# Kernel optimization log

Hardware: AMD Instinct MI355X
Metric: run time of the kernel (lower is better)

Reference implementation:

```python
import jax, jax.numpy as jnp
import numpy as np

H = 8       # n_heads
N = 128     # n_vars
HEAD = 64   # per-head dim (== __init__ dim)


def setup_inputs() -> dict:
    key = jax.random.key(0)
    k0, k1, k2, k3, k4 = jax.random.split(key, 5)
    B, L = 4, 8192
    D = H * HEAD
    x = jax.random.normal(k0, (B, L, D), dtype=jnp.float32)
    # nn.Linear default init: U(-1/sqrt(fan_in), 1/sqrt(fan_in)), fan_in = HEAD
    s = 1.0 / np.sqrt(HEAD)
    w1 = jax.random.uniform(k1, (HEAD, HEAD), jnp.float32, -s, s)
    b1 = jax.random.uniform(k2, (HEAD,), jnp.float32, -s, s)
    w2 = jax.random.uniform(k3, (HEAD, HEAD), jnp.float32, -s, s)
    b2 = jax.random.uniform(k4, (HEAD,), jnp.float32, -s, s)
    return {"x": x, "w1": w1, "b1": b1, "w2": w2, "b2": b2}


def reference(x, w1, b1, w2, b2):
    B, L, D = x.shape
    P = L // N  # patches per variable
    # (B,L,D) -> (B,H,L,HEAD) -> (B,H,N,P,HEAD)
    xh = x.reshape(B, L, H, HEAD).transpose(0, 2, 1, 3).reshape(B, H, N, P, HEAD)
    q = xh @ w1.T + b1  # proj_1
    k = xh @ w2.T + b2  # proj_2
    # per (b,h,patch) NxN adjacency over variables
    adj = jax.nn.gelu(jnp.einsum('bhixd,bhjxd->bhxij', q, k), approximate=False)
    adj = jax.nn.softmax(adj, axis=-1)
    # dropout is identity in eval mode; F.normalize(p=1): divide by max(L1, eps)
    adj = adj / jnp.maximum(jnp.sum(jnp.abs(adj), axis=-1, keepdims=True), 1e-12)
    out = jnp.einsum('bhxij,bhjxd->bixhd', adj, xh)  # (B,N,P,H,HEAD)
    return out.reshape(B, L, H * HEAD)
```

## Files before the change

kernel.cpp:

```cpp
#include <hip/hip_runtime.h>
#include <math.h>


namespace {
constexpr int H = 8, NV = 128, HEAD = 64, B = 4, L = 8192;
constexpr int P = L / NV;
constexpr int D = H * HEAD;
constexpr int RS = P * D;
constexpr int NT2 = (B * H * P) / 2;

constexpr int XT_S = 136;
constexpr int XH_S = 72;
constexpr int TA_S = 72;

typedef _Float16 half8  __attribute__((ext_vector_type(8)));
typedef _Float16 half4h __attribute__((ext_vector_type(4)));
typedef _Float16 half2v __attribute__((ext_vector_type(2)));
typedef float    floatx4 __attribute__((ext_vector_type(4)));

__device__ __forceinline__ floatx4 mfma16(half8 a, half8 b, floatx4 c) {
    return __builtin_amdgcn_mfma_f32_16x16x32_f16(a, b, c, 0, 0, 0);
}

__device__ __forceinline__ float& uslot(_Float16* xt, int j) {
    return ((float*)(xt + (j >> 2) * XT_S + 128))[j & 3];
}
__device__ __forceinline__ float& vslot(_Float16* xt, int j) {
    return ((float*)(xt + (32 + (j >> 2)) * XT_S + 128))[j & 3];
}

__global__ __launch_bounds__(256) void pack_g(
    const float* __restrict__ w1, const float* __restrict__ w2,
    const float* __restrict__ b1, const float* __restrict__ b2,
    _Float16* __restrict__ gxh, float* __restrict__ cf)
{
    const int t = threadIdx.x;
    if (blockIdx.x == 16) {
        for (int z = t; z < 14 * 64; z += 256) gxh[66 * 64 + z] = (_Float16)0.f;
        if (t < 64) {
            float a = 0.f;
            #pragma unroll 8
            for (int n = 0; n < 64; ++n) a = fmaf(w2[n * 64 + t], b1[n], a);
            gxh[64 * 64 + t] = (_Float16)a;
        } else if (t < 128) {
            const int d = t - 64;
            float a = 0.f;
            #pragma unroll 8
            for (int n = 0; n < 64; ++n) a = fmaf(w1[n * 64 + d], b2[n], a);
            gxh[65 * 64 + d] = (_Float16)a;
        } else if (t == 128) {
            float a = 0.f;
            for (int n = 0; n < 64; ++n) a = fmaf(b1[n], b2[n], a);
            cf[0] = a;
        }
        return;
    }
    const int gid = blockIdx.x * 256 + t;
    const int d = gid & 63, e = gid >> 6;
    float a = 0.f;
    #pragma unroll 8
    for (int n = 0; n < 64; ++n) a = fmaf(w1[n * 64 + d], w2[n * 64 + e], a);
    gxh[e * 64 + d] = (_Float16)a;
}

__global__ __launch_bounds__(256, 3) void space_graph_mfma9(
    const float* __restrict__ x, const _Float16* __restrict__ gxh,
    const float* __restrict__ cf, float* __restrict__ out)
{
    __shared__ _Float16 lds[64 * XT_S + NV * XH_S + NV * TA_S];
    _Float16* Xt = lds;
    _Float16* Xh = lds + 64 * XT_S;
    _Float16* TA = Xh + NV * XH_S;

    const int t    = threadIdx.x;
    const int lane = t & 63;
    const int w    = t >> 6;
    const int col  = lane & 15;
    const int quad = lane >> 4;
    const int c    = t & 15;
    const int ttv  = t >> 4;

    const int blk = blockIdx.x;
    const int ti0 = blk, ti1 = blk + NT2;
    const size_t base0 =
        ((size_t)(ti0 >> 9) * L + (size_t)(ti0 & (P - 1))) * D + (size_t)((ti0 >> 6) & (H - 1)) * HEAD;
    const size_t base1 =
        ((size_t)(ti1 >> 9) * L + (size_t)(ti1 & (P - 1))) * D + (size_t)((ti1 >> 6) & (H - 1)) * HEAD;

    const float cc = cf[0];

    float4 pf[8];
    #pragma unroll
    for (int it = 0; it < 4; ++it) {
        const int j0 = 2 * (ttv + 16 * it);
        pf[2 * it]     = *(const float4*)(x + base0 + (size_t)j0 * RS + c * 4);
        pf[2 * it + 1] = *(const float4*)(x + base0 + (size_t)(j0 + 1) * RS + c * 4);
    }

    #pragma unroll
    for (int tile = 0; tile < 2; ++tile) {
        const size_t base = (tile == 0) ? base0 : base1;

        if (tile == 1) {
            asm volatile("s_waitcnt lgkmcnt(0)" ::: "memory");
            __builtin_amdgcn_s_barrier();
            __builtin_amdgcn_sched_barrier(0);
        }

        #pragma unroll
        for (int it = 0; it < 4; ++it) {
            const int j0 = 2 * (ttv + 16 * it);
            const float4 v0 = pf[2 * it];
            const float4 v1 = pf[2 * it + 1];
            const float va[4] = {v0.x, v0.y, v0.z, v0.w};
            const float vb[4] = {v1.x, v1.y, v1.z, v1.w};
            half4h ra, rb;
            #pragma unroll
            for (int q = 0; q < 4; ++q) {
                const _Float16 ha = (_Float16)va[q];
                const _Float16 hb = (_Float16)vb[q];
                ra[q] = ha; rb[q] = hb;
                half2v pr; pr[0] = ha; pr[1] = hb;
                *(half2v*)&Xt[(4 * c + q) * XT_S + j0] = pr;
            }
            *(half4h*)&Xh[(size_t)j0 * XH_S + 4 * c] = ra;
            *(half4h*)&Xh[(size_t)(j0 + 1) * XH_S + 4 * c] = rb;
        }

        asm volatile("s_waitcnt lgkmcnt(0)" ::: "memory");
        __builtin_amdgcn_s_barrier();
        __builtin_amdgcn_sched_barrier(0);

        floatx4 tacc[2][5];
        #pragma unroll
        for (int mt = 0; mt < 2; ++mt)
            #pragma unroll
            for (int nt = 0; nt < 5; ++nt) tacc[mt][nt] = (floatx4)0.0f;

        half8 axf[2][2];
        #pragma unroll
        for (int ks = 0; ks < 2; ++ks)
            #pragma unroll
            for (int mt = 0; mt < 2; ++mt)
                axf[mt][ks] = *(const half8*)&Xh[(32 * w + 16 * mt + col) * XH_S + quad * 8 + 32 * ks];

        #pragma unroll
        for (int ks = 0; ks < 2; ++ks)
            #pragma unroll
            for (int nt = 0; nt < 5; ++nt) {
                const half8 gb8 = *(const half8*)&gxh[(col + 16 * nt) * HEAD + quad * 8 + 32 * ks];
                #pragma unroll
                for (int mt = 0; mt < 2; ++mt)
                    tacc[mt][nt] = mfma16(axf[mt][ks], gb8, tacc[mt][nt]);
            }

        #pragma unroll
        for (int mt = 0; mt < 2; ++mt)
            #pragma unroll
            for (int r = 0; r < 4; ++r) {
                const int R = 32 * w + 16 * mt + quad * 4 + r;
                if (col == 0) vslot(Xt, R) = tacc[mt][4][r];
                if (col == 1) uslot(Xt, R) = tacc[mt][4][r];
            }

        #pragma unroll
        for (int mt = 0; mt < 2; ++mt)
            #pragma unroll
            for (int r = 0; r < 4; ++r) {
                const int R = 32 * w + 16 * mt + quad * 4 + r;
                _Float16* trow = &TA[R * TA_S + col];
                #pragma unroll
                for (int nt = 0; nt < 4; ++nt)
                    trow[nt * 16] = (_Float16)(tacc[mt][nt][r]);
            }

        asm volatile("s_waitcnt lgkmcnt(0)" ::: "memory");
        __builtin_amdgcn_s_barrier();
        __builtin_amdgcn_sched_barrier(0);

        if (tile == 0) {
            #pragma unroll
            for (int it = 0; it < 4; ++it) {
                const int j0 = 2 * (ttv + 16 * it);
                pf[2 * it]     = *(const float4*)(x + base1 + (size_t)j0 * RS + c * 4);
                pf[2 * it + 1] = *(const float4*)(x + base1 + (size_t)(j0 + 1) * RS + c * 4);
            }
            __builtin_amdgcn_sched_barrier(0);
        }

        float ucr[2][4];
        #pragma unroll
        for (int mt = 0; mt < 2; ++mt)
            #pragma unroll
            for (int r = 0; r < 4; ++r)
                ucr[mt][r] = uslot(Xt, 32 * w + 16 * mt + quad * 4 + r) + cc;
        float vrow[8];
        #pragma unroll
        for (int nt = 0; nt < 8; ++nt) vrow[nt] = vslot(Xt, col + 16 * nt);

        floatx4 sacc[2][8];
        #pragma unroll
        for (int mt = 0; mt < 2; ++mt)
            #pragma unroll
            for (int nt = 0; nt < 8; ++nt)
                #pragma unroll
                for (int r = 0; r < 4; ++r)
                    sacc[mt][nt][r] = ucr[mt][r] + vrow[nt];

        #pragma unroll
        for (int ks = 0; ks < 2; ++ks) {
            half8 taf[2];
            #pragma unroll
            for (int mt = 0; mt < 2; ++mt)
                taf[mt] = *(const half8*)&TA[(32 * w + 16 * mt + col) * TA_S + quad * 8 + 32 * ks];
            #pragma unroll
            for (int nt = 0; nt < 8; ++nt) {
                const half8 xb = *(const half8*)&Xh[(col + 16 * nt) * XH_S + quad * 8 + 32 * ks];
                #pragma unroll
                for (int mt = 0; mt < 2; ++mt)
                    sacc[mt][nt] = mfma16(taf[mt], xb, sacc[mt][nt]);
            }
        }

        #pragma unroll
        for (int mt = 0; mt < 2; ++mt)
            #pragma unroll
            for (int r = 0; r < 4; ++r) {
                float wv[8]; float rs = 0.f;
                #pragma unroll
                for (int nt = 0; nt < 8; ++nt) {
                    const float s  = sacc[mt][nt][r];
                    const float pl = fmaf(s * s, -0.10294310f, -2.3022157f);
                    const float em = __builtin_amdgcn_exp2f(s * pl);
                    const float rr = __builtin_amdgcn_rcpf(1.0f + em);
                    const float e  = __builtin_amdgcn_exp2f((s * 1.44269504f) * rr);
                    wv[nt] = e; rs += e;
                }
                rs += __shfl_xor(rs, 1); rs += __shfl_xor(rs, 2);
                rs += __shfl_xor(rs, 4); rs += __shfl_xor(rs, 8);
                const float inv = __builtin_amdgcn_rcpf(rs);
                #pragma unroll
                for (int nt = 0; nt < 8; ++nt) sacc[mt][nt][r] = wv[nt] * inv;
            }

        #pragma unroll
        for (int mt = 0; mt < 2; ++mt)
            #pragma unroll
            for (int r = 0; r < 4; ++r) {
                const int R = 32 * w + 16 * mt + quad * 4 + r;
                _Float16* arow = &TA[R * TA_S + col];
                #pragma unroll
                for (int nt = 0; nt < 4; ++nt)
                    arow[nt * 16] = (_Float16)(sacc[mt][nt][r]);
            }

        floatx4 oacc[2][4];
        #pragma unroll
        for (int mt = 0; mt < 2; ++mt)
            #pragma unroll
            for (int nt = 0; nt < 4; ++nt) oacc[mt][nt] = (floatx4)0.0f;

        #pragma unroll
        for (int kh = 0; kh < 2; ++kh) {
            half8 aaf[2];
            #pragma unroll
            for (int mt = 0; mt < 2; ++mt)
                aaf[mt] = *(const half8*)&TA[(32 * w + 16 * mt + col) * TA_S + quad * 8 + 32 * kh];
            #pragma unroll
            for (int nt = 0; nt < 4; ++nt) {
                const half8 xb = *(const half8*)&Xt[(col + 16 * nt) * XT_S + quad * 8 + 32 * kh];
                #pragma unroll
                for (int mt = 0; mt < 2; ++mt)
                    oacc[mt][nt] = mfma16(aaf[mt], xb, oacc[mt][nt]);
            }
        }

        #pragma unroll
        for (int mt = 0; mt < 2; ++mt)
            #pragma unroll
            for (int r = 0; r < 4; ++r) {
                const int R = 32 * w + 16 * mt + quad * 4 + r;
                _Float16* arow = &TA[R * TA_S + col];
                #pragma unroll
                for (int nt = 4; nt < 8; ++nt)
                    arow[(nt - 4) * 16] = (_Float16)(sacc[mt][nt][r]);
            }

        #pragma unroll
        for (int kh = 0; kh < 2; ++kh) {
            half8 aaf[2];
            #pragma unroll
            for (int mt = 0; mt < 2; ++mt)
                aaf[mt] = *(const half8*)&TA[(32 * w + 16 * mt + col) * TA_S + quad * 8 + 32 * kh];
            #pragma unroll
            for (int nt = 0; nt < 4; ++nt) {
                const half8 xb = *(const half8*)&Xt[(col + 16 * nt) * XT_S + quad * 8 + 32 * (kh + 2)];
                #pragma unroll
                for (int mt = 0; mt < 2; ++mt)
                    oacc[mt][nt] = mfma16(aaf[mt], xb, oacc[mt][nt]);
            }
        }

        #pragma unroll
        for (int mt = 0; mt < 2; ++mt)
            #pragma unroll
            for (int r = 0; r < 4; ++r) {
                const int i = 32 * w + 16 * mt + quad * 4 + r;
                float* orow = out + base + (size_t)i * RS + col;
                #pragma unroll
                for (int nt = 0; nt < 4; ++nt)
                    orow[nt * 16] = oacc[mt][nt][r];
            }
    }
}
}

extern "C" void kernel_launch(void* const* d_in, const int* in_sizes, int n_in,
                              void* d_out, int out_size, void* d_ws, size_t ws_size,
                              hipStream_t stream) {
    const float* x  = (const float*)d_in[0];
    const float* w1 = (const float*)d_in[1];
    const float* b1 = (const float*)d_in[2];
    const float* w2 = (const float*)d_in[3];
    const float* b2 = (const float*)d_in[4];
    float* out = (float*)d_out;

    _Float16* gxh = (_Float16*)d_ws;
    float* cf = (float*)((char*)d_ws + 10240);

    hipLaunchKernelGGL(pack_g, dim3(17), dim3(256), 0, stream,
                       w1, w2, b1, b2, gxh, cf);
    hipLaunchKernelGGL(space_graph_mfma9, dim3(NT2), dim3(256), 0, stream,
                       x, gxh, cf, out);
}
```

Baseline: 158.7 us.

## Process one tile per block and load first-GEMM operands straight from global

Drops the two-tiles-per-block scheme with register prefetch of the second tile and launches one block per (b,h,patch) tile, doubling the grid. The A fragments for the first MFMA are now read directly from global memory and converted with packed round-toward-zero conversion, instead of being staged through LDS. This removes one block-wide barrier before the first GEMM. The trade-off is lost explicit overlap of the next tile's loads with compute, with the hardware scheduler across more blocks left to hide latency instead. x is also read twice from global, and rounding differs slightly from the LDS path.

```diff
diff --git a/kernel.cpp b/kernel.cpp
--- a/kernel.cpp
+++ b/kernel.cpp
@@ -7,7 +7,6 @@
 constexpr int P = L / NV;
 constexpr int D = H * HEAD;
 constexpr int RS = P * D;
-constexpr int NT2 = (B * H * P) / 2;
 
 constexpr int XT_S = 136;
 constexpr int XH_S = 72;
@@ -16,10 +15,24 @@
 typedef _Float16 half8  __attribute__((ext_vector_type(8)));
 typedef _Float16 half4h __attribute__((ext_vector_type(4)));
 typedef _Float16 half2v __attribute__((ext_vector_type(2)));
+typedef __fp16   fp16x2 __attribute__((ext_vector_type(2)));
 typedef float    floatx4 __attribute__((ext_vector_type(4)));
 
 __device__ __forceinline__ floatx4 mfma16(half8 a, half8 b, floatx4 c) {
     return __builtin_amdgcn_mfma_f32_16x16x32_f16(a, b, c, 0, 0, 0);
+}
+
+__device__ __forceinline__ half8 cvt8(float4 a, float4 b) {
+    fp16x2 p0 = __builtin_amdgcn_cvt_pkrtz(a.x, a.y);
+    fp16x2 p1 = __builtin_amdgcn_cvt_pkrtz(a.z, a.w);
+    fp16x2 p2 = __builtin_amdgcn_cvt_pkrtz(b.x, b.y);
+    fp16x2 p3 = __builtin_amdgcn_cvt_pkrtz(b.z, b.w);
+    half8 r;
+    r[0] = (_Float16)p0[0]; r[1] = (_Float16)p0[1];
+    r[2] = (_Float16)p1[0]; r[3] = (_Float16)p1[1];
+    r[4] = (_Float16)p2[0]; r[5] = (_Float16)p2[1];
+    r[6] = (_Float16)p3[0]; r[7] = (_Float16)p3[1];
+    return r;
 }
 
 __device__ __forceinline__ float& uslot(_Float16* xt, int j) {
@@ -63,7 +76,7 @@
     gxh[e * 64 + d] = (_Float16)a;
 }
 
-__global__ __launch_bounds__(256, 3) void space_graph_mfma9(
+__global__ __launch_bounds__(256, 3) void space_graph_mfma11(
     const float* __restrict__ x, const _Float16* __restrict__ gxh,
     const float* __restrict__ cf, float* __restrict__ out)
 {
@@ -77,41 +90,23 @@
     const int w    = t >> 6;
     const int col  = lane & 15;
     const int quad = lane >> 4;
-    const int c    = t & 15;
-    const int ttv  = t >> 4;
 
     const int blk = blockIdx.x;
-    const int ti0 = blk, ti1 = blk + NT2;
-    const size_t base0 =
-        ((size_t)(ti0 >> 9) * L + (size_t)(ti0 & (P - 1))) * D + (size_t)((ti0 >> 6) & (H - 1)) * HEAD;
-    const size_t base1 =
-        ((size_t)(ti1 >> 9) * L + (size_t)(ti1 & (P - 1))) * D + (size_t)((ti1 >> 6) & (H - 1)) * HEAD;
+    const int p = blk & (P - 1);
+    const int h = (blk >> 6) & (H - 1);
+    const int b = blk >> 9;
+    const size_t base = ((size_t)b * L + (size_t)p) * D + (size_t)h * HEAD;
 
     const float cc = cf[0];
 
-    float4 pf[8];
-    #pragma unroll
-    for (int it = 0; it < 4; ++it) {
-        const int j0 = 2 * (ttv + 16 * it);
-        pf[2 * it]     = *(const float4*)(x + base0 + (size_t)j0 * RS + c * 4);
-        pf[2 * it + 1] = *(const float4*)(x + base0 + (size_t)(j0 + 1) * RS + c * 4);
-    }
-
-    #pragma unroll
-    for (int tile = 0; tile < 2; ++tile) {
-        const size_t base = (tile == 0) ? base0 : base1;
-
-        if (tile == 1) {
-            asm volatile("s_waitcnt lgkmcnt(0)" ::: "memory");
-            __builtin_amdgcn_s_barrier();
-            __builtin_amdgcn_sched_barrier(0);
-        }
-
+    {
+        const int c  = t & 15;
+        const int tt = t >> 4;
         #pragma unroll
         for (int it = 0; it < 4; ++it) {
-            const int j0 = 2 * (ttv + 16 * it);
-            const float4 v0 = pf[2 * it];
-            const float4 v1 = pf[2 * it + 1];
+            const int j0 = 2 * (tt + 16 * it);
+            const float4 v0 = *(const float4*)(x + base + (size_t)j0 * RS + c * 4);
+            const float4 v1 = *(const float4*)(x + base + (size_t)(j0 + 1) * RS + c * 4);
             const float va[4] = {v0.x, v0.y, v0.z, v0.w};
             const float vb[4] = {v1.x, v1.y, v1.z, v1.w};
             half4h ra, rb;
@@ -126,192 +121,171 @@
             *(half4h*)&Xh[(size_t)j0 * XH_S + 4 * c] = ra;
             *(half4h*)&Xh[(size_t)(j0 + 1) * XH_S + 4 * c] = rb;
         }
-
-        asm volatile("s_waitcnt lgkmcnt(0)" ::: "memory");
-        __builtin_amdgcn_s_barrier();
-        __builtin_amdgcn_sched_barrier(0);
-
-        floatx4 tacc[2][5];
+    }
+
+    floatx4 tacc[2][5];
+    #pragma unroll
+    for (int mt = 0; mt < 2; ++mt)
+        #pragma unroll
+        for (int nt = 0; nt < 5; ++nt) tacc[mt][nt] = (floatx4)0.0f;
+
+    half8 axf[2][2];
+    #pragma unroll
+    for (int ks = 0; ks < 2; ++ks)
+        #pragma unroll
+        for (int mt = 0; mt < 2; ++mt) {
+            const int row = 32 * w + 16 * mt + col;
+            const float* src = x + base + (size_t)row * RS + quad * 8 + 32 * ks;
+            axf[mt][ks] = cvt8(*(const float4*)src, *(const float4*)(src + 4));
+        }
+
+    #pragma unroll
+    for (int ks = 0; ks < 2; ++ks)
+        #pragma unroll
+        for (int nt = 0; nt < 5; ++nt) {
+            const half8 gb8 = *(const half8*)&gxh[(col + 16 * nt) * HEAD + quad * 8 + 32 * ks];
+            #pragma unroll
+            for (int mt = 0; mt < 2; ++mt)
+                tacc[mt][nt] = mfma16(axf[mt][ks], gb8, tacc[mt][nt]);
+        }
+
+    #pragma unroll
+    for (int mt = 0; mt < 2; ++mt)
+        #pragma unroll
+        for (int r = 0; r < 4; ++r) {
+            const int R = 32 * w + 16 * mt + quad * 4 + r;
+            if (col == 0) vslot(Xt, R) = tacc[mt][4][r];
+            if (col == 1) uslot(Xt, R) = tacc[mt][4][r];
+            _Float16* trow = &TA[R * TA_S + col];
+            #pragma unroll
+            for (int nt = 0; nt < 4; ++nt)
+                trow[nt * 16] = (_Float16)(tacc[mt][nt][r]);
+        }
+    __syncthreads();
+
+    float ucr[2][4];
+    #pragma unroll
+    for (int mt = 0; mt < 2; ++mt)
+        #pragma unroll
+        for (int r = 0; r < 4; ++r)
+            ucr[mt][r] = uslot(Xt, 32 * w + 16 * mt + quad * 4 + r) + cc;
+    float vrow[8];
+    #pragma unroll
+    for (int nt = 0; nt < 8; ++nt) vrow[nt] = vslot(Xt, col + 16 * nt);
+
+    floatx4 sacc[2][8];
+    #pragma unroll
+    for (int mt = 0; mt < 2; ++mt)
+        #pragma unroll
+        for (int nt = 0; nt < 8; ++nt)
+            #pragma unroll
+            for (int r = 0; r < 4; ++r)
+                sacc[mt][nt][r] = ucr[mt][r] + vrow[nt];
+
+    #pragma unroll
+    for (int ks = 0; ks < 2; ++ks) {
+        half8 taf[2];
         #pragma unroll
         for (int mt = 0; mt < 2; ++mt)
-            #pragma unroll
-            for (int nt = 0; nt < 5; ++nt) tacc[mt][nt] = (floatx4)0.0f;
-
-        half8 axf[2][2];
-        #pragma unroll
-        for (int ks = 0; ks < 2; ++ks)
+            taf[mt] = *(const half8*)&TA[(32 * w + 16 * mt + col) * TA_S + quad * 8 + 32 * ks];
+        #pragma unroll
+        for (int nt = 0; nt < 8; ++nt) {
+            const half8 xb = *(const half8*)&Xh[(col + 16 * nt) * XH_S + quad * 8 + 32 * ks];
             #pragma unroll
             for (int mt = 0; mt < 2; ++mt)
-                axf[mt][ks] = *(const half8*)&Xh[(32 * w + 16 * mt + col) * XH_S + quad * 8 + 32 * ks];
-
-        #pragma unroll
-        for (int ks = 0; ks < 2; ++ks)
-            #pragma unroll
-            for (int nt = 0; nt < 5; ++nt) {
-                const half8 gb8 = *(const half8*)&gxh[(col + 16 * nt) * HEAD + quad * 8 + 32 * ks];
-                #pragma unroll
-                for (int mt = 0; mt < 2; ++mt)
-                    tacc[mt][nt] = mfma16(axf[mt][ks], gb8, tacc[mt][nt]);
+                sacc[mt][nt] = mfma16(taf[mt], xb, sacc[mt][nt]);
+        }
+    }
+
+    #pragma unroll
+    for (int mt = 0; mt < 2; ++mt)
+        #pragma unroll
+        for (int r = 0; r < 4; ++r) {
+            float wv[8]; float rs = 0.f;
+            #pragma unroll
+            for (int nt = 0; nt < 8; ++nt) {
+                const float s  = sacc[mt][nt][r];
+                const float pl = fmaf(s * s, -0.10294310f, -2.3022157f);
+                const float em = __builtin_amdgcn_exp2f(s * pl);
+                const float rr = __builtin_amdgcn_rcpf(1.0f + em);
+                const float e  = __builtin_amdgcn_exp2f((s * 1.44269504f) * rr);
+                wv[nt] = e; rs += e;
             }
-
+            rs += __shfl_xor(rs, 1); rs += __shfl_xor(rs, 2);
+            rs += __shfl_xor(rs, 4); rs += __shfl_xor(rs, 8);
+            const float inv = __builtin_amdgcn_rcpf(rs);
+            #pragma unroll
+            for (int nt = 0; nt < 8; ++nt) sacc[mt][nt][r] = wv[nt] * inv;
+        }
+
+    #pragma unroll
+    for (int mt = 0; mt < 2; ++mt)
+        #pragma unroll
+        for (int r = 0; r < 4; ++r) {
+            const int R = 32 * w + 16 * mt + quad * 4 + r;
+            _Float16* arow = &TA[R * TA_S + col];
+            #pragma unroll
+            for (int nt = 0; nt < 4; ++nt)
+                arow[nt * 16] = (_Float16)(sacc[mt][nt][r]);
+        }
+
+    floatx4 oacc[2][4];
+    #pragma unroll
+    for (int mt = 0; mt < 2; ++mt)
+        #pragma unroll
+        for (int nt = 0; nt < 4; ++nt) oacc[mt][nt] = (floatx4)0.0f;
+
+    #pragma unroll
+    for (int kh = 0; kh < 2; ++kh) {
+        half8 aaf[2];
         #pragma unroll
         for (int mt = 0; mt < 2; ++mt)
-            #pragma unroll
-            for (int r = 0; r < 4; ++r) {
-                const int R = 32 * w + 16 * mt + quad * 4 + r;
-                if (col == 0) vslot(Xt, R) = tacc[mt][4][r];
-                if (col == 1) uslot(Xt, R) = tacc[mt][4][r];
-            }
-
+            aaf[mt] = *(const half8*)&TA[(32 * w + 16 * mt + col) * TA_S + quad * 8 + 32 * kh];
+        #pragma unroll
+        for (int nt = 0; nt < 4; ++nt) {
+            const half8 xb = *(const half8*)&Xt[(col + 16 * nt) * XT_S + quad * 8 + 32 * kh];
+            #pragma unroll
+            for (int mt = 0; mt < 2; ++mt)
+                oacc[mt][nt] = mfma16(aaf[mt], xb, oacc[mt][nt]);
+        }
+    }
+
+    #pragma unroll
+    for (int mt = 0; mt < 2; ++mt)
+        #pragma unroll
+        for (int r = 0; r < 4; ++r) {
+            const int R = 32 * w + 16 * mt + quad * 4 + r;
+            _Float16* arow = &TA[R * TA_S + col];
+            #pragma unroll
+            for (int nt = 4; nt < 8; ++nt)
+                arow[(nt - 4) * 16] = (_Float16)(sacc[mt][nt][r]);
+        }
+
+    #pragma unroll
+    for (int kh = 0; kh < 2; ++kh) {
+        half8 aaf[2];
         #pragma unroll
         for (int mt = 0; mt < 2; ++mt)
-            #pragma unroll
-            for (int r = 0; r < 4; ++r) {
-                const int R = 32 * w + 16 * mt + quad * 4 + r;
-                _Float16* trow = &TA[R * TA_S + col];
-                #pragma unroll
-                for (int nt = 0; nt < 4; ++nt)
-                    trow[nt * 16] = (_Float16)(tacc[mt][nt][r]);
-            }
-
-        asm volatile("s_waitcnt lgkmcnt(0)" ::: "memory");
-        __builtin_amdgcn_s_barrier();
-        __builtin_amdgcn_sched_barrier(0);
-
-        if (tile == 0) {
-            #pragma unroll
-            for (int it = 0; it < 4; ++it) {
-                const int j0 = 2 * (ttv + 16 * it);
-                pf[2 * it]     = *(const float4*)(x + base1 + (size_t)j0 * RS + c * 4);
-                pf[2 * it + 1] = *(const float4*)(x + base1 + (size_t)(j0 + 1) * RS + c * 4);
-            }
-            __builtin_amdgcn_sched_barrier(0);
-        }
-
-        float ucr[2][4];
-        #pragma unroll
-        for (int mt = 0; mt < 2; ++mt)
-            #pragma unroll
-            for (int r = 0; r < 4; ++r)
-                ucr[mt][r] = uslot(Xt, 32 * w + 16 * mt + quad * 4 + r) + cc;
-        float vrow[8];
-        #pragma unroll
-        for (int nt = 0; nt < 8; ++nt) vrow[nt] = vslot(Xt, col + 16 * nt);
-
-        floatx4 sacc[2][8];
-        #pragma unroll
-        for (int mt = 0; mt < 2; ++mt)
-            #pragma unroll
-            for (int nt = 0; nt < 8; ++nt)
-                #pragma unroll
-                for (int r = 0; r < 4; ++r)
-                    sacc[mt][nt][r] = ucr[mt][r] + vrow[nt];
-
-        #pragma unroll
-        for (int ks = 0; ks < 2; ++ks) {
-            half8 taf[2];
+            aaf[mt] = *(const half8*)&TA[(32 * w + 16 * mt + col) * TA_S + quad * 8 + 32 * kh];
+        #pragma unroll
+        for (int nt = 0; nt < 4; ++nt) {
+            const half8 xb = *(const half8*)&Xt[(col + 16 * nt) * XT_S + quad * 8 + 32 * (kh + 2)];
             #pragma unroll
             for (int mt = 0; mt < 2; ++mt)
-                taf[mt] = *(const half8*)&TA[(32 * w + 16 * mt + col) * TA_S + quad * 8 + 32 * ks];
-            #pragma unroll
-            for (int nt = 0; nt < 8; ++nt) {
-                const half8 xb = *(const half8*)&Xh[(col + 16 * nt) * XH_S + quad * 8 + 32 * ks];
-                #pragma unroll
-                for (int mt = 0; mt < 2; ++mt)
-                    sacc[mt][nt] = mfma16(taf[mt], xb, sacc[mt][nt]);
-            }
-        }
-
-        #pragma unroll
-        for (int mt = 0; mt < 2; ++mt)
-            #pragma unroll
-            for (int r = 0; r < 4; ++r) {
-                float wv[8]; float rs = 0.f;
-                #pragma unroll
-                for (int nt = 0; nt < 8; ++nt) {
-                    const float s  = sacc[mt][nt][r];
-                    const float pl = fmaf(s * s, -0.10294310f, -2.3022157f);
-                    const float em = __builtin_amdgcn_exp2f(s * pl);
-                    const float rr = __builtin_amdgcn_rcpf(1.0f + em);
-                    const float e  = __builtin_amdgcn_exp2f((s * 1.44269504f) * rr);
-                    wv[nt] = e; rs += e;
-                }
-                rs += __shfl_xor(rs, 1); rs += __shfl_xor(rs, 2);
-                rs += __shfl_xor(rs, 4); rs += __shfl_xor(rs, 8);
-                const float inv = __builtin_amdgcn_rcpf(rs);
-                #pragma unroll
-                for (int nt = 0; nt < 8; ++nt) sacc[mt][nt][r] = wv[nt] * inv;
-            }
-
-        #pragma unroll
-        for (int mt = 0; mt < 2; ++mt)
-            #pragma unroll
-            for (int r = 0; r < 4; ++r) {
-                const int R = 32 * w + 16 * mt + quad * 4 + r;
-                _Float16* arow = &TA[R * TA_S + col];
-                #pragma unroll
-                for (int nt = 0; nt < 4; ++nt)
-                    arow[nt * 16] = (_Float16)(sacc[mt][nt][r]);
-            }
-
-        floatx4 oacc[2][4];
-        #pragma unroll
-        for (int mt = 0; mt < 2; ++mt)
-            #pragma unroll
-            for (int nt = 0; nt < 4; ++nt) oacc[mt][nt] = (floatx4)0.0f;
-
-        #pragma unroll
-        for (int kh = 0; kh < 2; ++kh) {
-            half8 aaf[2];
-            #pragma unroll
-            for (int mt = 0; mt < 2; ++mt)
-                aaf[mt] = *(const half8*)&TA[(32 * w + 16 * mt + col) * TA_S + quad * 8 + 32 * kh];
-            #pragma unroll
-            for (int nt = 0; nt < 4; ++nt) {
-                const half8 xb = *(const half8*)&Xt[(col + 16 * nt) * XT_S + quad * 8 + 32 * kh];
-                #pragma unroll
-                for (int mt = 0; mt < 2; ++mt)
-                    oacc[mt][nt] = mfma16(aaf[mt], xb, oacc[mt][nt]);
-            }
-        }
-
-        #pragma unroll
-        for (int mt = 0; mt < 2; ++mt)
-            #pragma unroll
-            for (int r = 0; r < 4; ++r) {
-                const int R = 32 * w + 16 * mt + quad * 4 + r;
-                _Float16* arow = &TA[R * TA_S + col];
-                #pragma unroll
-                for (int nt = 4; nt < 8; ++nt)
-                    arow[(nt - 4) * 16] = (_Float16)(sacc[mt][nt][r]);
-            }
-
-        #pragma unroll
-        for (int kh = 0; kh < 2; ++kh) {
-            half8 aaf[2];
-            #pragma unroll
-            for (int mt = 0; mt < 2; ++mt)
-                aaf[mt] = *(const half8*)&TA[(32 * w + 16 * mt + col) * TA_S + quad * 8 + 32 * kh];
-            #pragma unroll
-            for (int nt = 0; nt < 4; ++nt) {
-                const half8 xb = *(const half8*)&Xt[(col + 16 * nt) * XT_S + quad * 8 + 32 * (kh + 2)];
-                #pragma unroll
-                for (int mt = 0; mt < 2; ++mt)
-                    oacc[mt][nt] = mfma16(aaf[mt], xb, oacc[mt][nt]);
-            }
-        }
-
-        #pragma unroll
-        for (int mt = 0; mt < 2; ++mt)
-            #pragma unroll
-            for (int r = 0; r < 4; ++r) {
-                const int i = 32 * w + 16 * mt + quad * 4 + r;
-                float* orow = out + base + (size_t)i * RS + col;
-                #pragma unroll
-                for (int nt = 0; nt < 4; ++nt)
-                    orow[nt * 16] = oacc[mt][nt][r];
-            }
-    }
+                oacc[mt][nt] = mfma16(aaf[mt], xb, oacc[mt][nt]);
+        }
+    }
+
+    #pragma unroll
+    for (int mt = 0; mt < 2; ++mt)
+        #pragma unroll
+        for (int r = 0; r < 4; ++r) {
+            const int i = 32 * w + 16 * mt + quad * 4 + r;
+            float* orow = out + base + (size_t)i * RS + col;
+            #pragma unroll
+            for (int nt = 0; nt < 4; ++nt)
+                orow[nt * 16] = oacc[mt][nt][r];
+        }
 }
 }
 
@@ -330,6 +304,6 @@
 
     hipLaunchKernelGGL(pack_g, dim3(17), dim3(256), 0, stream,
                        w1, w2, b1, b2, gxh, cf);
-    hipLaunchKernelGGL(space_graph_mfma9, dim3(NT2), dim3(256), 0, stream,
+    hipLaunchKernelGGL(space_graph_mfma11, dim3(B * H * P), dim3(256), 0, stream,
                        x, gxh, cf, out);
 }
```

Result: faster. 141.3 us (-11.0%).
